# Kernel tuning notes

Hardware: AMD Instinct MI355X
Metric: run time of the kernel (lower is better)

The kernel has to match this reference:

```python
import jax, jax.numpy as jnp
import numpy as np
from jax import lax

NUM_C = 100
EMB = 256
B = 64
L = 500
NSTU = 4096
N = NUM_C + 1  # skill_embedding rows / GCN node count


def gcn_conv(x, src, dst, W, b):
    # PyG GCNConv: add self-loops, symmetric deg^-1/2 norm, scatter-add at target.
    # x: [N, Fin]; src, dst: [E] (duplicates kept, as in PyG); W: [Fout, Fin]
    n = x.shape[0]
    loop = jnp.arange(n)
    s = jnp.concatenate([src, loop])
    d = jnp.concatenate([dst, loop])
    deg = jnp.zeros((n,), x.dtype).at[d].add(1.0)
    dinv = jnp.where(deg > 0, lax.rsqrt(deg), 0.0)
    norm = dinv[s] * dinv[d]  # [E+N]
    h = x @ W.T
    out = jnp.zeros((n, h.shape[1]), x.dtype).at[d].add(norm[:, None] * h[s])
    return out + b


def rnn(x, Wih, Whh, bih, bhh):
    # torch.nn.RNN (tanh, batch_first): h_t = tanh(x_t Wih^T + bih + h_{t-1} Whh^T + bhh)
    h0 = jnp.zeros((x.shape[0], Whh.shape[0]), x.dtype)
    def step(h, xt):
        h = jnp.tanh(xt @ Wih.T + bih + h @ Whh.T + bhh)
        return h, h
    _, hs = lax.scan(step, h0, jnp.swapaxes(x, 0, 1))
    return jnp.swapaxes(hs, 0, 1)


def next_pred(res, skill):
    # (res * one_hot(next_skill)).sum(-1); row NUM_C of the one-hot table is all-zero padding
    ns = skill[:, 1:]
    p = jnp.take_along_axis(res, jnp.minimum(ns, NUM_C - 1)[..., None], axis=-1)[..., 0]
    return jnp.where(ns == NUM_C, 0.0, p)


def _forward(student, skill, answer, G, skill_emb, answer_emb, stu,
             hg_w1, hg_b1, hg_w2, hg_b2, gcn_w1, gcn_b1, gcn_w2, gcn_b2,
             w1_w, w1_b, w2_w, w2_b, fc_d_w, fc_d_b, fc_h_w, fc_h_b,
             fc_e_w, fc_e_b, pos, dg_wih, dg_whh, dg_bih, dg_bhh,
             hgr_wih, hgr_whh, hgr_bih, hgr_bhh):
    mask = (answer != 2)[..., None].astype(jnp.float32)  # [B,L,1]
    src, dst = skill[:, :-1], skill[:, 1:]               # per-sample edge lists [B,L-1]

    # HGNN over student hypergraph (eval mode: dropout = identity): x' = G (x W + b)
    h = jax.nn.relu(G @ (stu @ hg_w1.T + hg_b1))
    stu_embedding = G @ (h @ hg_w2.T + hg_b2)            # [NSTU, EMB]

    se = skill_emb[skill]                                # [B,L,EMB]
    ae = answer_emb[answer]
    skill_answer = jnp.concatenate([se, ae], -1)
    answer_skill = jnp.concatenate([ae, se], -1)
    stu_h = stu_embedding[student - 1]                   # one_hot @ table == gather, [B,L,EMB]

    # per-sample 2-layer GCN over the shared skill embedding table, vmapped over batch
    gcn2 = jax.vmap(lambda s, d: gcn_conv(
        jax.nn.relu(gcn_conv(skill_emb, s, d, gcn_w1, gcn_b1)), s, d, gcn_w2, gcn_b2))
    all_h = gcn2(src, dst)                               # [B,N,EMB]

    g = jnp.take_along_axis(all_h, skill[..., None], axis=1) * mask  # [B,L,EMB]
    lengths = mask.sum(axis=1)[:, 0].astype(jnp.int32)   # effective lengths [B]
    expand_pos = pos[lengths - 1]                        # [B,L,1] (L==500)
    expand_pos = jax.nn.softmax(expand_pos * mask, axis=1)
    pooled = (g * expand_pos).sum(axis=1)                # [B,EMB]
    pooled = jnp.broadcast_to(pooled[:, None, :], (B, L, EMB))

    x = jnp.where((answer == 1)[..., None], skill_answer, answer_skill)  # [B,L,2E]
    h_dg = rnn(jnp.concatenate([pooled, x], -1), dg_wih, dg_whh, dg_bih, dg_bhh)
    h_hg = rnn(jnp.concatenate([stu_h, x], -1), hgr_wih, hgr_whh, hgr_bih, hgr_bhh)

    logit_h = h_hg @ fc_h_w.T + fc_h_b
    logit_d = h_dg @ fc_d_w.T + fc_d_b
    theta = jax.nn.sigmoid(h_hg @ w1_w.T + w1_b + h_dg @ w2_w.T + w2_b)
    ens = jnp.concatenate([theta * h_hg, (1.0 - theta) * h_dg], -1) @ fc_e_w.T + fc_e_b
    return (next_pred(logit_h[:, :-1], skill),
            next_pred(logit_d[:, :-1], skill),
            next_pred(ens[:, :-1], skill))


def setup_inputs() -> dict:
    key = jax.random.key(0)
    ks = jax.random.split(key, 24)
    f = lambda i, shape, s=0.05: jax.random.normal(ks[i], shape, jnp.float32) * s
    return {
        "student": jax.random.randint(ks[0], (B, L), 1, NSTU + 1),
        "skill": jax.random.randint(ks[1], (B, L), 0, N),
        "answer": jax.random.randint(ks[2], (B, L), 0, 3),
        "G": f(3, (NSTU, NSTU), 0.01),
        "skill_emb": f(4, (N, EMB), 1.0),
        "answer_emb": f(5, (3, EMB), 1.0),
        "stu": f(6, (NSTU, EMB), 1.0),
        "hg_w1": f(7, (EMB, EMB)), "hg_b1": jnp.zeros((EMB,), jnp.float32),
        "hg_w2": f(8, (EMB, EMB)), "hg_b2": jnp.zeros((EMB,), jnp.float32),
        "gcn_w1": f(9, (8, EMB)), "gcn_b1": jnp.zeros((8,), jnp.float32),
        "gcn_w2": f(10, (EMB, 8)), "gcn_b2": jnp.zeros((EMB,), jnp.float32),
        "w1_w": f(11, (EMB, EMB)), "w1_b": jnp.zeros((EMB,), jnp.float32),
        "w2_w": f(12, (EMB, EMB)), "w2_b": jnp.zeros((EMB,), jnp.float32),
        "fc_d_w": f(13, (NUM_C, EMB)), "fc_d_b": jnp.zeros((NUM_C,), jnp.float32),
        "fc_h_w": f(14, (NUM_C, EMB)), "fc_h_b": jnp.zeros((NUM_C,), jnp.float32),
        "fc_e_w": f(15, (NUM_C, 2 * EMB)), "fc_e_b": jnp.zeros((NUM_C,), jnp.float32),
        "pos": jax.random.uniform(ks[16], (500, 500, 1), jnp.float32),
        "dg_wih": f(17, (EMB, 3 * EMB)), "dg_whh": f(18, (EMB, EMB)),
        "dg_bih": jnp.zeros((EMB,), jnp.float32), "dg_bhh": jnp.zeros((EMB,), jnp.float32),
        "hgr_wih": f(19, (EMB, 3 * EMB)), "hgr_whh": f(20, (EMB, EMB)),
        "hgr_bih": jnp.zeros((EMB,), jnp.float32), "hgr_bhh": jnp.zeros((EMB,), jnp.float32),
    }


def reference(student, skill, answer, G, skill_emb, answer_emb, stu,
              hg_w1, hg_b1, hg_w2, hg_b2, gcn_w1, gcn_b1, gcn_w2, gcn_b2,
              w1_w, w1_b, w2_w, w2_b, fc_d_w, fc_d_b, fc_h_w, fc_h_b,
              fc_e_w, fc_e_b, pos, dg_wih, dg_whh, dg_bih, dg_bhh,
              hgr_wih, hgr_whh, hgr_bih, hgr_bhh):
    return _forward(student, skill, answer, G, skill_emb, answer_emb, stu,
                    hg_w1, hg_b1, hg_w2, hg_b2, gcn_w1, gcn_b1, gcn_w2, gcn_b2,
                    w1_w, w1_b, w2_w, w2_b, fc_d_w, fc_d_b, fc_h_w, fc_h_b,
                    fc_e_w, fc_e_b, pos, dg_wih, dg_whh, dg_bih, dg_bhh,
                    hgr_wih, hgr_whh, hgr_bih, hgr_bhh)
```

## Files before the change

### kernel.cpp

```cpp
#include <hip/hip_runtime.h>
#include <cstdint>
#include <cstddef>

typedef unsigned short u16;
typedef __attribute__((ext_vector_type(8))) short short8;
typedef __attribute__((ext_vector_type(4))) short short4v;
typedef __attribute__((ext_vector_type(4))) float f32x4;

__device__ __forceinline__ float b2f(u16 u){ return __uint_as_float(((unsigned)u)<<16); }
__device__ __forceinline__ u16 f2b(float f){
    unsigned u = __float_as_uint(f);
    return (u16)((u + 0x7fffu + ((u>>16)&1u)) >> 16);
}
__device__ __forceinline__ int iclamp(int v, int lo, int hi){ return v<lo?lo:(v>hi?hi:v); }

__device__ __forceinline__ void barrier_lds(){
    asm volatile("s_waitcnt lgkmcnt(0)\n\ts_barrier" ::: "memory");
}

__device__ __forceinline__ float fast_exp2(float x){
#if __has_builtin(__builtin_amdgcn_exp2f)
    return __builtin_amdgcn_exp2f(x);
#else
    return __expf(x * 0.6931471805599453f);
#endif
}

__device__ __forceinline__ short8 ld8f(const float* p){
    f32x4 a = *(const f32x4*)p;
    f32x4 b = *(const f32x4*)(p+4);
    short8 r;
    #pragma unroll
    for(int j=0;j<4;j++){ r[j]=(short)f2b(a[j]); r[4+j]=(short)f2b(b[j]); }
    return r;
}
__device__ __forceinline__ short8 ld8f_s(const float* p, float s){
    f32x4 a = *(const f32x4*)p;
    f32x4 b = *(const f32x4*)(p+4);
    short8 r;
    #pragma unroll
    for(int j=0;j<4;j++){ r[j]=(short)f2b(a[j]*s); r[4+j]=(short)f2b(b[j]*s); }
    return r;
}
__device__ __forceinline__ short8 ld8b(const u16* p){ return *(const short8*)p; }

#define C_TANH 2.8853900817779268f

__global__ __launch_bounds__(256) void k_cvt(const float* __restrict__ in, u16* __restrict__ outp){
    const size_t i = ((size_t)blockIdx.x*256 + threadIdx.x)*8;
    *(short8*)&outp[i] = ld8f(in + i);
}

template<bool TRANSOUT, bool RELU, bool AF32, bool BF32>
__global__ __launch_bounds__(256) void gemm64(
    const void* __restrict__ A, const void* __restrict__ B,
    const float* __restrict__ bias, u16* __restrict__ C,
    int M, int N, int K, int ldb, int ldc)
{
    constexpr int BK=32;
    __shared__ u16 As[64][BK+8];
    __shared__ u16 Bs[64][BK+8];
    const int tid = threadIdx.x;
    const int bm = blockIdx.x*64, bn = blockIdx.y*64;
    const int wave = tid>>6, lane = tid&63, lm = lane&15, lg = lane>>4;
    const int wm = (wave>>1)*32, wn = (wave&1)*32;
    f32x4 acc[2][2];
    #pragma unroll
    for(int i=0;i<2;i++){ acc[i][0]=(f32x4){0.f,0.f,0.f,0.f}; acc[i][1]=(f32x4){0.f,0.f,0.f,0.f}; }

    const int arow = tid>>2, akc = (tid&3)*8;
    for(int k0=0;k0<K;k0+=BK){
        *(short8*)&As[arow][akc] = AF32 ? ld8f((const float*)A + (size_t)(bm+arow)*K + k0+akc)
                                        : ld8b((const u16*)A + (size_t)(bm+arow)*K + k0+akc);
        *(short8*)&Bs[arow][akc] = BF32 ? ld8f((const float*)B + (size_t)(bn+arow)*ldb + k0+akc)
                                        : ld8b((const u16*)B + (size_t)(bn+arow)*ldb + k0+akc);
        __syncthreads();
        short8 af[2], bfg[2];
        #pragma unroll
        for(int mt=0;mt<2;mt++) af[mt]  = *(const short8*)&As[wm+mt*16+lm][lg*8];
        #pragma unroll
        for(int nt=0;nt<2;nt++) bfg[nt] = *(const short8*)&Bs[wn+nt*16+lm][lg*8];
        #pragma unroll
        for(int nt=0;nt<2;nt++)
            #pragma unroll
            for(int mt=0;mt<2;mt++)
                acc[mt][nt] = __builtin_amdgcn_mfma_f32_16x16x32_bf16(af[mt], bfg[nt], acc[mt][nt], 0,0,0);
        __syncthreads();
    }
    #pragma unroll
    for(int nt=0;nt<2;nt++){
        const int col = bn+wn+nt*16+lm;
        const float bv = bias ? bias[col] : 0.f;
        #pragma unroll
        for(int mt=0;mt<2;mt++){
            const int row0 = bm+wm+mt*16+lg*4;
            #pragma unroll
            for(int r=0;r<4;r++){
                const int row = row0+r;
                float v = acc[mt][nt][r] + bv;
                if(RELU) v = fmaxf(v, 0.f);
                const size_t idx = TRANSOUT ? ((size_t)col*ldc + row) : ((size_t)row*ldc + col);
                C[idx] = f2b(v);
            }
        }
    }
}

__global__ __launch_bounds__(256) void k_h1pre(const float* __restrict__ skill_emb,
                                               const float* __restrict__ gcn_w1,
                                               float* __restrict__ h1pre)
{
    const int i = blockIdx.x*101 + threadIdx.x;
    if(threadIdx.x >= 101) return;
    const int idx = i; if(idx>=808) return;
    const int n=idx>>3, j=idx&7;
    const float* x = skill_emb + n*256;
    const float* w = gcn_w1 + j*256;
    float acc=0.f;
    for(int k=0;k<256;k+=4){
        f32x4 a = *(const f32x4*)&x[k];
        f32x4 b = *(const f32x4*)&w[k];
        acc += a.x*b.x + a.y*b.y + a.z*b.z + a.w*b.w;
    }
    h1pre[idx]=acc;
}

__global__ __launch_bounds__(256) void k_idx(const int* __restrict__ skill,
                                             const int* __restrict__ answer,
                                             const int* __restrict__ student,
                                             int* __restrict__ combo_t, int* __restrict__ sid_t)
{
    const int i = blockIdx.x*256 + threadIdx.x;
    if(i>=32000) return;
    const int t = i>>6, b = i&63;
    const int sk = iclamp(skill[b*500+t], 0, 100);
    const int an = iclamp(answer[b*500+t], 0, 2);
    const int sd = iclamp(student[b*500+t]-1, 0, 4095);
    combo_t[i] = sk*3+an;
    sid_t[i]   = sd;
}

__global__ __launch_bounds__(256) void k_gcn(
    const int* __restrict__ skill, const int* __restrict__ answer,
    const float* __restrict__ pos, const float* __restrict__ h1pre,
    const float* __restrict__ gcn_b1, const float* __restrict__ gcn_w2, const float* __restrict__ gcn_b2,
    float* __restrict__ pooled)
{
    const int b = blockIdx.x, tid = threadIdx.x;
    __shared__ int   sk[500];
    __shared__ float msk[500];
    __shared__ float coef[500];
    __shared__ float deg[101];
    __shared__ float agg1[101*8];
    __shared__ float agg2[101*8];
    __shared__ float red[256];
    __shared__ float vec8[8];
    __shared__ float sS[1];

    for(int i=tid;i<500;i+=256){
        sk[i]=iclamp(skill[b*500+i],0,100);
        msk[i] = (answer[b*500+i]!=2)?1.f:0.f;
    }
    for(int i=tid;i<101;i+=256) deg[i]=1.f;
    if(tid<8)  vec8[tid]=0.f;
    if(tid==8) sS[0]=0.f;
    __syncthreads();
    for(int e=tid;e<499;e+=256) atomicAdd(&deg[sk[e+1]], 1.f);
    __syncthreads();
    for(int i=tid;i<101;i+=256) deg[i] = rsqrtf(deg[i]);
    float cnt=0.f; for(int i=tid;i<500;i+=256) cnt += msk[i];
    __syncthreads();
    red[tid]=cnt; __syncthreads();
    for(int s=128;s>0;s>>=1){ if(tid<s) red[tid]+=red[tid+s]; __syncthreads(); }
    const int len = iclamp((int)(red[0]+0.5f), 1, 500);
    __syncthreads();
    for(int i=tid;i<808;i+=256){ const int n=i>>3; agg1[i] = deg[n]*deg[n]*h1pre[i]; }
    __syncthreads();
    for(int i=tid;i<499*8;i+=256){
        const int e=i>>3, j=i&7, s=sk[e], d=sk[e+1];
        atomicAdd(&agg1[d*8+j], deg[s]*deg[d]*h1pre[s*8+j]);
    }
    __syncthreads();
    for(int i=tid;i<808;i+=256){ const int j=i&7; agg1[i] = fmaxf(agg1[i]+gcn_b1[j], 0.f); }
    __syncthreads();
    for(int i=tid;i<808;i+=256){ const int n=i>>3; agg2[i] = deg[n]*deg[n]*agg1[i]; }
    __syncthreads();
    for(int i=tid;i<499*8;i+=256){
        const int e=i>>3, j=i&7, s=sk[e], d=sk[e+1];
        atomicAdd(&agg2[d*8+j], deg[s]*deg[d]*agg1[s*8+j]);
    }
    const size_t prow = (size_t)(len-1)*500;
    float vmax = -1e30f;
    for(int i=tid;i<500;i+=256){ const float v = pos[prow+i]*msk[i]; coef[i]=v; vmax=fmaxf(vmax,v); }
    red[tid]=vmax; __syncthreads();
    for(int s=128;s>0;s>>=1){ if(tid<s) red[tid]=fmaxf(red[tid],red[tid+s]); __syncthreads(); }
    const float m = red[0]; __syncthreads();
    float lsum=0.f;
    for(int i=tid;i<500;i+=256){ const float e=__expf(coef[i]-m); coef[i]=e; lsum+=e; }
    red[tid]=lsum; __syncthreads();
    for(int s=128;s>0;s>>=1){ if(tid<s) red[tid]+=red[tid+s]; __syncthreads(); }
    const float inv = 1.f/red[0];
    __syncthreads();
    float v8[8]={0,0,0,0,0,0,0,0}; float ls=0.f;
    for(int i=tid;i<500;i+=256){
        const float ci = coef[i]*inv*msk[i];
        if(ci!=0.f){
            const int n=sk[i]; ls+=ci;
            #pragma unroll
            for(int j=0;j<8;j++) v8[j] += ci*agg2[n*8+j];
        }
    }
    #pragma unroll
    for(int j=0;j<8;j++) atomicAdd(&vec8[j], v8[j]);
    atomicAdd(&sS[0], ls);
    __syncthreads();
    {
        const int o = tid;
        float acc = gcn_b2[o]*sS[0];
        #pragma unroll
        for(int j=0;j<8;j++) acc += vec8[j]*gcn_w2[o*8+j];
        pooled[b*256+o] = acc;
    }
}

__global__ __launch_bounds__(256) void k_table(
    const float* __restrict__ skill_emb, const float* __restrict__ answer_emb,
    const float* __restrict__ wih, const float* __restrict__ bih, const float* __restrict__ bhh,
    float* __restrict__ table)
{
    const int combo = blockIdx.x, tid = threadIdx.x;
    const int sid = combo/3, ans = combo - sid*3;
    __shared__ float sf[256], sg[256];
    sf[tid] = (ans==1) ? skill_emb[(size_t)sid*256+tid] : answer_emb[(size_t)ans*256+tid];
    sg[tid] = (ans==1) ? answer_emb[(size_t)ans*256+tid] : skill_emb[(size_t)sid*256+tid];
    __syncthreads();
    const int o = tid;
    float acc = bih[o] + bhh[o];
    const float* w = wih + (size_t)o*768;
    for(int k=0;k<256;k+=4){
        f32x4 w1v = *(const f32x4*)&w[256+k];
        f32x4 w2v = *(const f32x4*)&w[512+k];
        acc += sf[k]*w1v.x + sf[k+1]*w1v.y + sf[k+2]*w1v.z + sf[k+3]*w1v.w;
        acc += sg[k]*w2v.x + sg[k+1]*w2v.y + sg[k+2]*w2v.z + sg[k+3]*w2v.w;
    }
    table[(size_t)combo*256 + o] = acc;
}

__global__ __launch_bounds__(256) void k_pooledproj(const float* __restrict__ pooled,
                                                    const float* __restrict__ wih,
                                                    u16* __restrict__ outp)
{
    const int b=blockIdx.x, tid=threadIdx.x;
    __shared__ float p[256];
    p[tid] = pooled[b*256+tid];
    __syncthreads();
    const float* w = wih + (size_t)tid*768;
    float acc=0.f;
    for(int k=0;k<256;k+=4){
        f32x4 wv = *(const f32x4*)&w[k];
        acc += p[k]*wv.x + p[k+1]*wv.y + p[k+2]*wv.z + p[k+3]*wv.w;
    }
    outp[b*256+tid]=f2b(acc);
}

__global__ __launch_bounds__(256) void k_pre(
    const int* __restrict__ combo_t, const int* __restrict__ sid_t,
    const float* __restrict__ table_dg, const float* __restrict__ table_hg,
    const u16* __restrict__ pooled_proj, const u16* __restrict__ stu_proj,
    u16* __restrict__ pre_dg, u16* __restrict__ pre_hg)
{
    const int t = blockIdx.x, rnn = blockIdx.y, c = threadIdx.x;
    const int b0 = blockIdx.z*16;
    const float* tab = rnn ? table_hg : table_dg;
    u16* outp = rnn ? pre_hg : pre_dg;
    for(int b=b0;b<b0+16;b++){
        const int cmb = combo_t[t*64+b];
        const u16* prow = rnn ? (stu_proj + (size_t)sid_t[t*64+b]*256)
                              : (pooled_proj + (size_t)b*256);
        const float v = (tab[(size_t)cmb*256 + c] + b2f(prow[c])) * C_TANH;
        outp[((size_t)t*64+b)*256 + c] = f2b(v);
    }
}

__global__ __launch_bounds__(512) void k_rnn(
    const u16* __restrict__ pre_dg, const u16* __restrict__ pre_hg,
    const float* __restrict__ whh_dg, const float* __restrict__ whh_hg,
    u16* __restrict__ hall_dg, u16* __restrict__ hall_hg)
{
    __shared__ u16 hc[2][8][4][16][8];
    const int bid = blockIdx.x;
    const int rnn = bid>>2, grp = bid&3, rb = grp*16;
    const float* W   = rnn ? whh_hg : whh_dg;
    const u16*  pre  = rnn ? pre_hg : pre_dg;
    u16*        out  = rnn ? hall_hg : hall_dg;
    const int tid = threadIdx.x, wave = tid>>6, lane = tid&63;
    const int lm = lane&15, lg = lane>>4;
    const int cb = wave*32;

    short8 wf[2][8];
    #pragma unroll
    for(int nt=0;nt<2;nt++)
        #pragma unroll
        for(int kk=0;kk<8;kk++)
            wf[nt][kk] = ld8f_s(W + (size_t)(cb+nt*16+lm)*256 + kk*32 + lg*8, C_TANH);

    for(int i=tid;i<2*8*4*16*8/2;i+=512) ((unsigned*)hc)[i]=0;

    const size_t base = (size_t)(rb+lm)*256 + cb + lg*4;
    const int wsub = lg>>1, wslot = (lg&1)*4;

    const u16* pp = pre + base;
    u16*       op = out + base;
    uint2 pv0 = *(const uint2*)pp;
    uint2 pv1 = *(const uint2*)(pp+16);
    pp += 16384;
    __syncthreads();

    auto stepf = [&](const u16 (&S)[8][4][16][8], u16 (&D)[8][4][16][8]){
        f32x4 a0, a1, c0, c1;
        a0[0] = __uint_as_float(pv0.x << 16);
        a0[1] = __uint_as_float(pv0.x & 0xffff0000u);
        a0[2] = __uint_as_float(pv0.y << 16);
        a0[3] = __uint_as_float(pv0.y & 0xffff0000u);
        a1[0] = __uint_as_float(pv1.x << 16);
        a1[1] = __uint_as_float(pv1.x & 0xffff0000u);
        a1[2] = __uint_as_float(pv1.y << 16);
        a1[3] = __uint_as_float(pv1.y & 0xffff0000u);
        c0 = (f32x4){0.f,0.f,0.f,0.f};
        c1 = (f32x4){0.f,0.f,0.f,0.f};
        #pragma unroll
        for(int kk=0;kk<4;kk++){
            short8 hb = *(const short8*)&S[kk][lg][lm][0];
            a0 = __builtin_amdgcn_mfma_f32_16x16x32_bf16(wf[0][kk], hb, a0, 0,0,0);
            a1 = __builtin_amdgcn_mfma_f32_16x16x32_bf16(wf[1][kk], hb, a1, 0,0,0);
        }
        #pragma unroll
        for(int kk=4;kk<8;kk++){
            short8 hb = *(const short8*)&S[kk][lg][lm][0];
            c0 = __builtin_amdgcn_mfma_f32_16x16x32_bf16(wf[0][kk], hb, c0, 0,0,0);
            c1 = __builtin_amdgcn_mfma_f32_16x16x32_bf16(wf[1][kk], hb, c1, 0,0,0);
        }
        const uint2 pn0 = *(const uint2*)pp;
        const uint2 pn1 = *(const uint2*)(pp+16);
        float th[8];
        #pragma unroll
        for(int r=0;r<4;r++){
            const float x0 = a0[r] + c0[r];
            const float x1 = a1[r] + c1[r];
            th[r]   = fmaf(-2.f, __builtin_amdgcn_rcpf(fast_exp2(x0) + 1.f), 1.f);
            th[4+r] = fmaf(-2.f, __builtin_amdgcn_rcpf(fast_exp2(x1) + 1.f), 1.f);
        }
        uint2 pk0, pk1;
        asm("v_cvt_pk_bf16_f32 %0, %1, %2" : "=v"(pk0.x) : "v"(th[0]), "v"(th[1]));
        asm("v_cvt_pk_bf16_f32 %0, %1, %2" : "=v"(pk0.y) : "v"(th[2]), "v"(th[3]));
        asm("v_cvt_pk_bf16_f32 %0, %1, %2" : "=v"(pk1.x) : "v"(th[4]), "v"(th[5]));
        asm("v_cvt_pk_bf16_f32 %0, %1, %2" : "=v"(pk1.y) : "v"(th[6]), "v"(th[7]));
        *(uint2*)&D[wave][wsub  ][lm][wslot] = pk0;
        *(uint2*)&D[wave][wsub+2][lm][wslot] = pk1;
        *(uint2*)op      = pk0;
        *(uint2*)(op+16) = pk1;
        barrier_lds();
        pv0 = pn0; pv1 = pn1;
    };

    for(int t=0;t<500;t+=2){
        stepf(hc[0], hc[1]);  pp += 16384; op += 16384;
        stepf(hc[1], hc[0]);  pp += 16384; op += 16384;
    }
}

__global__ __launch_bounds__(256) void k_theta(
    const u16* __restrict__ Ah, const u16* __restrict__ Ad,
    const float* __restrict__ w1, const float* __restrict__ w2,
    const float* __restrict__ b1, const float* __restrict__ b2,
    u16* __restrict__ theta)
{
    constexpr int BK=32;
    __shared__ u16 AsH[128][BK+8];
    __shared__ u16 AsD[128][BK+8];
    __shared__ u16 BsH[64][BK+8];
    __shared__ u16 BsD[64][BK+8];
    const int tid = threadIdx.x;
    const int bm = blockIdx.x*128, bn = blockIdx.y*64;
    const int wave = tid>>6, lane = tid&63, lm = lane&15, lg = lane>>4;
    const int wm = (wave>>1)*64, wn = (wave&1)*32;
    f32x4 acc[4][2];
    #pragma unroll
    for(int i=0;i<4;i++){ acc[i][0]=(f32x4){0.f,0.f,0.f,0.f}; acc[i][1]=(f32x4){0.f,0.f,0.f,0.f}; }

    const int arow0 = tid>>2, akc0 = (tid&3)*8;
    const int arow1 = arow0 + 64;
    for(int k0=0;k0<256;k0+=BK){
        *(short8*)&AsH[arow0][akc0] = ld8b(Ah + (size_t)(bm+arow0)*256 + k0+akc0);
        *(short8*)&AsH[arow1][akc0] = ld8b(Ah + (size_t)(bm+arow1)*256 + k0+akc0);
        *(short8*)&AsD[arow0][akc0] = ld8b(Ad + (size_t)(bm+arow0)*256 + k0+akc0);
        *(short8*)&AsD[arow1][akc0] = ld8b(Ad + (size_t)(bm+arow1)*256 + k0+akc0);
        *(short8*)&BsH[arow0][akc0] = ld8f(w1 + (size_t)(bn+arow0)*256 + k0+akc0);
        *(short8*)&BsD[arow0][akc0] = ld8f(w2 + (size_t)(bn+arow0)*256 + k0+akc0);
        __syncthreads();
        short8 afH[4], afD[4], bf1[2], bf2[2];
        #pragma unroll
        for(int mt=0;mt<4;mt++){
            afH[mt] = *(const short8*)&AsH[wm+mt*16+lm][lg*8];
            afD[mt] = *(const short8*)&AsD[wm+mt*16+lm][lg*8];
        }
        #pragma unroll
        for(int nt=0;nt<2;nt++){
            bf1[nt] = *(const short8*)&BsH[wn+nt*16+lm][lg*8];
            bf2[nt] = *(const short8*)&BsD[wn+nt*16+lm][lg*8];
        }
        #pragma unroll
        for(int nt=0;nt<2;nt++)
            #pragma unroll
            for(int mt=0;mt<4;mt++){
                acc[mt][nt] = __builtin_amdgcn_mfma_f32_16x16x32_bf16(afH[mt], bf1[nt], acc[mt][nt], 0,0,0);
                acc[mt][nt] = __builtin_amdgcn_mfma_f32_16x16x32_bf16(afD[mt], bf2[nt], acc[mt][nt], 0,0,0);
            }
        __syncthreads();
    }
    #pragma unroll
    for(int nt=0;nt<2;nt++){
        const int col = bn+wn+nt*16+lm;
        const float bb = b1[col]+b2[col];
        #pragma unroll
        for(int mt=0;mt<4;mt++){
            const int row0 = bm+wm+mt*16+lg*4;
            #pragma unroll
            for(int r=0;r<4;r++){
                const float x = acc[mt][nt][r] + bb;
                theta[(size_t)(row0+r)*256 + col] = f2b(1.f/(1.f+__expf(-x)));
            }
        }
    }
}

__global__ __launch_bounds__(256) void k_out(
    const int* __restrict__ skill,
    const u16* __restrict__ hall_hg, const u16* __restrict__ hall_dg,
    const u16* __restrict__ theta,
    const float* __restrict__ fc_h_w, const float* __restrict__ fc_h_b,
    const float* __restrict__ fc_d_w, const float* __restrict__ fc_d_b,
    const float* __restrict__ fc_e_w, const float* __restrict__ fc_e_b,
    float* __restrict__ outp)
{
    const int tid=threadIdx.x, lane=tid&63;
    const int wid = blockIdx.x*4 + (tid>>6);
    const int b = wid/499, t = wid - b*499;
    const int ns = skill[b*500 + t + 1];
    float o0=0.f,o1=0.f,o2=0.f,bh=0.f,bd=0.f,be=0.f;
    if(ns != 100){
        const int c = iclamp(ns, 0, 99);
        const size_t r = (size_t)t*64 + b;
        const int k = lane*4;
        short4v hh  = *(const short4v*)&hall_hg[r*256+k];
        short4v hd  = *(const short4v*)&hall_dg[r*256+k];
        short4v th  = *(const short4v*)&theta[r*256+k];
        f32x4 fh  = *(const f32x4*)&fc_h_w[(size_t)c*256+k];
        f32x4 fd  = *(const f32x4*)&fc_d_w[(size_t)c*256+k];
        f32x4 fe1 = *(const f32x4*)&fc_e_w[(size_t)c*512+k];
        f32x4 fe2 = *(const f32x4*)&fc_e_w[(size_t)c*512+256+k];
        #pragma unroll
        for(int j=0;j<4;j++){
            const float hhj=b2f((u16)hh[j]), hdj=b2f((u16)hd[j]), tj=b2f((u16)th[j]);
            o0 += hhj*fh[j];
            o1 += hdj*fd[j];
            o2 += tj*hhj*fe1[j] + (1.f-tj)*hdj*fe2[j];
        }
        #pragma unroll
        for(int off=32;off>0;off>>=1){
            o0 += __shfl_down(o0,off);
            o1 += __shfl_down(o1,off);
            o2 += __shfl_down(o2,off);
        }
        bh=fc_h_b[c]; bd=fc_d_b[c]; be=fc_e_b[c];
    }
    if(lane==0){
        outp[            b*499+t] = (ns==100)?0.f:(o0+bh);
        outp[31936     + b*499+t] = (ns==100)?0.f:(o1+bd);
        outp[2*31936   + b*499+t] = (ns==100)?0.f:(o2+be);
    }
}

extern "C" void kernel_launch(void* const* d_in, const int* in_sizes, int n_in,
                              void* d_out, int out_size, void* d_ws, size_t ws_size,
                              hipStream_t stream)
{
    const int* student = (const int*)d_in[0];
    const int* skill   = (const int*)d_in[1];
    const int* answer  = (const int*)d_in[2];
    const float* G        = (const float*)d_in[3];
    const float* skill_emb= (const float*)d_in[4];
    const float* answer_emb=(const float*)d_in[5];
    const float* stu      = (const float*)d_in[6];
    const float* hg_w1    = (const float*)d_in[7];
    const float* hg_b1    = (const float*)d_in[8];
    const float* hg_w2    = (const float*)d_in[9];
    const float* hg_b2    = (const float*)d_in[10];
    const float* gcn_w1   = (const float*)d_in[11];
    const float* gcn_b1   = (const float*)d_in[12];
    const float* gcn_w2   = (const float*)d_in[13];
    const float* gcn_b2   = (const float*)d_in[14];
    const float* w1_w     = (const float*)d_in[15];
    const float* w1_b     = (const float*)d_in[16];
    const float* w2_w     = (const float*)d_in[17];
    const float* w2_b     = (const float*)d_in[18];
    const float* fc_d_w   = (const float*)d_in[19];
    const float* fc_d_b   = (const float*)d_in[20];
    const float* fc_h_w   = (const float*)d_in[21];
    const float* fc_h_b   = (const float*)d_in[22];
    const float* fc_e_w   = (const float*)d_in[23];
    const float* fc_e_b   = (const float*)d_in[24];
    const float* pos      = (const float*)d_in[25];
    const float* dg_wih   = (const float*)d_in[26];
    const float* dg_whh   = (const float*)d_in[27];
    const float* dg_bih   = (const float*)d_in[28];
    const float* dg_bhh   = (const float*)d_in[29];
    const float* hgr_wih  = (const float*)d_in[30];
    const float* hgr_whh  = (const float*)d_in[31];
    const float* hgr_bih  = (const float*)d_in[32];
    const float* hgr_bhh  = (const float*)d_in[33];

    char* ws = (char*)d_ws;
    size_t off = 0;
    auto nxt = [&](size_t bytes)->char*{
        char* r = ws + off;
        off += (bytes + 255) & ~(size_t)255;
        return r;
    };
    float* h1pre      = (float*)nxt(808*4);
    float* pooled     = (float*)nxt(64*256*4);
    float* table_dg   = (float*)nxt(303*256*4);
    float* table_hg   = (float*)nxt(303*256*4);
    u16*   tmpT       = (u16*)  nxt((size_t)256*4096*2);
    u16*   hbuf       = (u16*)  nxt((size_t)4096*256*2);
    u16*   stu_proj   = (u16*)  nxt((size_t)4096*256*2);
    u16*   pooled_proj= (u16*)  nxt(64*256*2);
    int*   combo_t    = (int*)  nxt(32000*4);
    int*   sid_t      = (int*)  nxt(32000*4);
    u16*   Gb         = (u16*)  nxt((size_t)4096*4096*2);
    u16*   hall_dg    = (u16*)  nxt((size_t)32000*256*2);
    u16*   hall_hg    = (u16*)  nxt((size_t)32000*256*2);
    u16*   pre_dg     = Gb;
    u16*   pre_hg     = Gb + (size_t)32000*256;
    u16*   theta      = pre_dg;

    k_h1pre<<<8,256,0,stream>>>(skill_emb, gcn_w1, h1pre);
    k_gcn<<<64,256,0,stream>>>(skill, answer, pos, h1pre, gcn_b1, gcn_w2, gcn_b2, pooled);
    k_table<<<303,256,0,stream>>>(skill_emb, answer_emb, dg_wih,  dg_bih,  dg_bhh,  table_dg);
    k_table<<<303,256,0,stream>>>(skill_emb, answer_emb, hgr_wih, hgr_bih, hgr_bhh, table_hg);
    k_idx<<<125,256,0,stream>>>(skill, answer, student, combo_t, sid_t);
    k_cvt<<<8192,256,0,stream>>>(G, Gb);

    gemm64<true ,false,true ,true ><<<dim3(64,4),256,0,stream>>>(stu,  hg_w1, hg_b1, tmpT, 4096,256,256,  256, 4096);
    gemm64<false,true ,false,false><<<dim3(64,4),256,0,stream>>>(Gb,   tmpT,  nullptr, hbuf, 4096,256,4096, 4096, 256);
    gemm64<true ,false,false,true ><<<dim3(64,4),256,0,stream>>>(hbuf, hg_w2, hg_b2, tmpT, 4096,256,256,  256, 4096);
    gemm64<false,false,false,false><<<dim3(64,4),256,0,stream>>>(Gb,   tmpT,  nullptr, hbuf, 4096,256,4096, 4096, 256);
    gemm64<false,false,false,true ><<<dim3(64,4),256,0,stream>>>(hbuf, hgr_wih, nullptr, stu_proj, 4096,256,256, 768, 256);

    k_pooledproj<<<64,256,0,stream>>>(pooled, dg_wih, pooled_proj);

    k_pre<<<dim3(500,2,4),256,0,stream>>>(combo_t, sid_t, table_dg, table_hg,
                                          pooled_proj, stu_proj, pre_dg, pre_hg);

    k_rnn<<<8,512,0,stream>>>(pre_dg, pre_hg, dg_whh, hgr_whh, hall_dg, hall_hg);

    k_theta<<<dim3(250,4),256,0,stream>>>(hall_hg, hall_dg, w1_w, w2_w, w1_b, w2_b, theta);
    k_out<<<7984,256,0,stream>>>(skill, hall_hg, hall_dg, theta,
                                 fc_h_w, fc_h_b, fc_d_w, fc_d_b, fc_e_w, fc_e_b,
                                 (float*)d_out);
}
```

Baseline: 850.5 us.

## Use 128-row GEMM tiles for G products and prefetch RNN inputs two steps ahead

Adds a gemm128 kernel with 128x64 block tiles and switches the two large G-matrix GEMMs and the stu_proj GEMM to it, halving the grid so each block reuses B tiles across more rows. The RNN recurrence now keeps two register buffers of precomputed inputs and issues each load a full step earlier, before the MFMA chain, to hide global memory latency on the serial critical path. The larger tile increases register use per thread, and with only 128 blocks on a chip with many compute units it may leave units idle.

```diff
diff --git a/kernel.cpp b/kernel.cpp
--- a/kernel.cpp
+++ b/kernel.cpp
@@ -101,6 +101,62 @@
                 if(RELU) v = fmaxf(v, 0.f);
                 const size_t idx = TRANSOUT ? ((size_t)col*ldc + row) : ((size_t)row*ldc + col);
                 C[idx] = f2b(v);
+            }
+        }
+    }
+}
+
+template<bool RELU, bool AF32, bool BF32>
+__global__ __launch_bounds__(256) void gemm128(
+    const void* __restrict__ A, const void* __restrict__ B,
+    const float* __restrict__ bias, u16* __restrict__ C,
+    int M, int N, int K, int ldb, int ldc)
+{
+    constexpr int BK=32;
+    __shared__ u16 As[128][BK+8];
+    __shared__ u16 Bs[64][BK+8];
+    const int tid = threadIdx.x;
+    const int bm = blockIdx.x*128, bn = blockIdx.y*64;
+    const int wave = tid>>6, lane = tid&63, lm = lane&15, lg = lane>>4;
+    const int wm = (wave>>1)*64, wn = (wave&1)*32;
+    f32x4 acc[4][2];
+    #pragma unroll
+    for(int i=0;i<4;i++){ acc[i][0]=(f32x4){0.f,0.f,0.f,0.f}; acc[i][1]=(f32x4){0.f,0.f,0.f,0.f}; }
+
+    const int arow0 = tid>>2, akc0 = (tid&3)*8;
+    const int arow1 = arow0 + 64;
+    for(int k0=0;k0<K;k0+=BK){
+        *(short8*)&As[arow0][akc0] = AF32 ? ld8f((const float*)A + (size_t)(bm+arow0)*K + k0+akc0)
+                                          : ld8b((const u16*)A + (size_t)(bm+arow0)*K + k0+akc0);
+        *(short8*)&As[arow1][akc0] = AF32 ? ld8f((const float*)A + (size_t)(bm+arow1)*K + k0+akc0)
+                                          : ld8b((const u16*)A + (size_t)(bm+arow1)*K + k0+akc0);
+        *(short8*)&Bs[arow0][akc0] = BF32 ? ld8f((const float*)B + (size_t)(bn+arow0)*ldb + k0+akc0)
+                                          : ld8b((const u16*)B + (size_t)(bn+arow0)*ldb + k0+akc0);
+        __syncthreads();
+        short8 af[4], bfg[2];
+        #pragma unroll
+        for(int mt=0;mt<4;mt++) af[mt]  = *(const short8*)&As[wm+mt*16+lm][lg*8];
+        #pragma unroll
+        for(int nt=0;nt<2;nt++) bfg[nt] = *(const short8*)&Bs[wn+nt*16+lm][lg*8];
+        #pragma unroll
+        for(int nt=0;nt<2;nt++)
+            #pragma unroll
+            for(int mt=0;mt<4;mt++)
+                acc[mt][nt] = __builtin_amdgcn_mfma_f32_16x16x32_bf16(af[mt], bfg[nt], acc[mt][nt], 0,0,0);
+        __syncthreads();
+    }
+    #pragma unroll
+    for(int nt=0;nt<2;nt++){
+        const int col = bn+wn+nt*16+lm;
+        const float bv = bias ? bias[col] : 0.f;
+        #pragma unroll
+        for(int mt=0;mt<4;mt++){
+            const int row0 = bm+wm+mt*16+lg*4;
+            #pragma unroll
+            for(int r=0;r<4;r++){
+                float v = acc[mt][nt][r] + bv;
+                if(RELU) v = fmaxf(v, 0.f);
+                C[(size_t)(row0+r)*ldc + col] = f2b(v);
             }
         }
     }
@@ -311,12 +367,15 @@
 
     const u16* pp = pre + base;
     u16*       op = out + base;
-    uint2 pv0 = *(const uint2*)pp;
-    uint2 pv1 = *(const uint2*)(pp+16);
-    pp += 16384;
-    __syncthreads();
-
-    auto stepf = [&](const u16 (&S)[8][4][16][8], u16 (&D)[8][4][16][8]){
+    uint2 pvA0 = *(const uint2*)pp;
+    uint2 pvA1 = *(const uint2*)(pp+16);
+    uint2 pvB0 = *(const uint2*)(pp+16384);
+    uint2 pvB1 = *(const uint2*)(pp+16384+16);
+    pp += 2*16384;
+    __syncthreads();
+
+    auto stepf = [&](const u16 (&S)[8][4][16][8], u16 (&D)[8][4][16][8],
+                     uint2& pv0, uint2& pv1){
         f32x4 a0, a1, c0, c1;
         a0[0] = __uint_as_float(pv0.x << 16);
         a0[1] = __uint_as_float(pv0.x & 0xffff0000u);
@@ -328,6 +387,8 @@
         a1[3] = __uint_as_float(pv1.y & 0xffff0000u);
         c0 = (f32x4){0.f,0.f,0.f,0.f};
         c1 = (f32x4){0.f,0.f,0.f,0.f};
+        pv0 = *(const uint2*)pp;
+        pv1 = *(const uint2*)(pp+16);
         #pragma unroll
         for(int kk=0;kk<4;kk++){
             short8 hb = *(const short8*)&S[kk][lg][lm][0];
@@ -340,8 +401,6 @@
             c0 = __builtin_amdgcn_mfma_f32_16x16x32_bf16(wf[0][kk], hb, c0, 0,0,0);
             c1 = __builtin_amdgcn_mfma_f32_16x16x32_bf16(wf[1][kk], hb, c1, 0,0,0);
         }
-        const uint2 pn0 = *(const uint2*)pp;
-        const uint2 pn1 = *(const uint2*)(pp+16);
         float th[8];
         #pragma unroll
         for(int r=0;r<4;r++){
@@ -360,12 +419,11 @@
         *(uint2*)op      = pk0;
         *(uint2*)(op+16) = pk1;
         barrier_lds();
-        pv0 = pn0; pv1 = pn1;
     };
 
     for(int t=0;t<500;t+=2){
-        stepf(hc[0], hc[1]);  pp += 16384; op += 16384;
-        stepf(hc[1], hc[0]);  pp += 16384; op += 16384;
+        stepf(hc[0], hc[1], pvA0, pvA1);  pp += 16384; op += 16384;
+        stepf(hc[1], hc[0], pvB0, pvB1);  pp += 16384; op += 16384;
     }
 }
 
@@ -551,11 +609,11 @@
     k_idx<<<125,256,0,stream>>>(skill, answer, student, combo_t, sid_t);
     k_cvt<<<8192,256,0,stream>>>(G, Gb);
 
-    gemm64<true ,false,true ,true ><<<dim3(64,4),256,0,stream>>>(stu,  hg_w1, hg_b1, tmpT, 4096,256,256,  256, 4096);
-    gemm64<false,true ,false,false><<<dim3(64,4),256,0,stream>>>(Gb,   tmpT,  nullptr, hbuf, 4096,256,4096, 4096, 256);
-    gemm64<true ,false,false,true ><<<dim3(64,4),256,0,stream>>>(hbuf, hg_w2, hg_b2, tmpT, 4096,256,256,  256, 4096);
-    gemm64<false,false,false,false><<<dim3(64,4),256,0,stream>>>(Gb,   tmpT,  nullptr, hbuf, 4096,256,4096, 4096, 256);
-    gemm64<false,false,false,true ><<<dim3(64,4),256,0,stream>>>(hbuf, hgr_wih, nullptr, stu_proj, 4096,256,256, 768, 256);
+    gemm64 <true ,false,true ,true ><<<dim3(64,4),256,0,stream>>>(stu,  hg_w1, hg_b1, tmpT, 4096,256,256,  256, 4096);
+    gemm128<true ,false,false><<<dim3(32,4),256,0,stream>>>(Gb,   tmpT,  nullptr, hbuf, 4096,256,4096, 4096, 256);
+    gemm64 <true ,false,false,true ><<<dim3(64,4),256,0,stream>>>(hbuf, hg_w2, hg_b2, tmpT, 4096,256,256,  256, 4096);
+    gemm128<false,false,false><<<dim3(32,4),256,0,stream>>>(Gb,   tmpT,  nullptr, hbuf, 4096,256,4096, 4096, 256);
+    gemm128<false,false,true ><<<dim3(32,4),256,0,stream>>>(hbuf, hgr_wih, nullptr, stu_proj, 4096,256,256, 768, 256);
 
     k_pooledproj<<<64,256,0,stream>>>(pooled, dg_wih, pooled_proj);
 
```

Result: slower. 901.2 us (+6.0%).
